# Optimization experiments

Measured on AMD Instinct MI355X. Metric: run time of the kernel, lower is better.

Reference implementation:

```python
import jax, jax.numpy as jnp
import numpy as np

B, T, D_IN, H, D_OUT = 64, 512, 512, 1024, 512

def setup_inputs() -> dict:
    key = jax.random.key(0)
    ks = jax.random.split(key, 8)
    s = 0.02  # weight init scale to keep gates in a sane range
    return {
        "x": jax.random.normal(ks[0], (B, T, D_IN), jnp.float32),
        "hx": jax.random.normal(ks[1], (B, H), jnp.float32) * 0.1,
        "cx": jax.random.normal(ks[2], (B, H), jnp.float32) * 0.1,
        "yx": jax.nn.softmax(jax.random.normal(ks[3], (B, D_OUT), jnp.float32), axis=-1),
        "Wi": jax.random.normal(ks[4], (4 * H, D_IN), jnp.float32) * s,
        "bi": jnp.zeros((4 * H,), jnp.float32),
        "Wh": jax.random.normal(ks[5], (4 * H, H), jnp.float32) * s,
        "bh": jnp.zeros((4 * H,), jnp.float32),
        "Wp": jax.random.normal(ks[6], (4 * H, D_OUT), jnp.float32) * s,
        "bp": jnp.zeros((4 * H,), jnp.float32),
        "Wo": jax.random.normal(ks[7], (D_OUT, H), jnp.float32) * s,
        "bo": jnp.zeros((D_OUT,), jnp.float32),
    }

def reference(x, hx, cx, yx, Wi, bi, Wh, bh, Wp, bp, Wo, bo):
    # Precompute input projections for all timesteps: [T, B, 4H]
    xg = jnp.einsum("btd,gd->tbg", x, Wi) + bi

    def step(carry, xg_t):
        h, c, y = carry
        gates = xg_t + h @ Wh.T + bh + y @ Wp.T + bp  # [B, 4H]
        i_g, f_g, g_g, o_g = jnp.split(gates, 4, axis=-1)
        i_g = jax.nn.sigmoid(i_g)
        f_g = jax.nn.sigmoid(f_g)
        g_g = jnp.tanh(g_g)
        o_g = jax.nn.sigmoid(o_g)
        c_new = f_g * c + i_g * g_g
        h_new = o_g * jnp.tanh(c_new)
        y_new = jax.nn.softmax(h_new @ Wo.T + bo, axis=-1)  # softmax feedback
        return (h_new, c_new, y_new), (h_new, y_new)

    (hT, cT, yT), (h_seq, y_seq) = jax.lax.scan(step, (hx, cx, yx), xg)
    output = jnp.transpose(h_seq, (1, 0, 2))       # [B, T, H]   (batch_first)
    output_peep = jnp.transpose(y_seq, (1, 0, 2))  # [B, T, D_OUT]
    return output, output_peep, hT, cT, yT
```

## Files before the change

kernel.cpp:

```cpp
#include <hip/hip_runtime.h>
#include <math.h>


typedef __bf16 bf16;
typedef bf16  bf16x8 __attribute__((ext_vector_type(8)));
typedef float f32x4  __attribute__((ext_vector_type(4)));
typedef unsigned long long u64;
typedef unsigned int u32;

#define B_    64
#define T_    512
#define DIN_  512
#define H_    1024
#define DOUT_ 512
#define NBLK  256
#define NTHR  512
#define GBLK  64
#define GROWS 16

__device__ __forceinline__ bf16x8 ld8f(const float* __restrict__ p) {
  const float4 a = *(const float4*)p;
  const float4 b = *(const float4*)(p + 4);
  bf16x8 r;
  r[0]=(bf16)a.x; r[1]=(bf16)a.y; r[2]=(bf16)a.z; r[3]=(bf16)a.w;
  r[4]=(bf16)b.x; r[5]=(bf16)b.y; r[6]=(bf16)b.z; r[7]=(bf16)b.w;
  return r;
}

__device__ __forceinline__ float sigm(float x){ return 1.f/(1.f+__expf(-x)); }

__device__ __forceinline__ void st_u64(void* p, u64 v) {
  __hip_atomic_store((u64*)p, v, __ATOMIC_RELAXED, __HIP_MEMORY_SCOPE_AGENT);
}
__device__ __forceinline__ u64 ld_u64(const void* p) {
  return __hip_atomic_load((const u64*)p, __ATOMIC_RELAXED, __HIP_MEMORY_SCOPE_AGENT);
}
__device__ __forceinline__ void st_u32(void* p, u32 v) {
  __hip_atomic_store((u32*)p, v, __ATOMIC_RELAXED, __HIP_MEMORY_SCOPE_AGENT);
}
__device__ __forceinline__ u32 ld_u32(const void* p) {
  return __hip_atomic_load((const u32*)p, __ATOMIC_RELAXED, __HIP_MEMORY_SCOPE_AGENT);
}
__device__ __forceinline__ void st_f32(float* p, float v) {
  __hip_atomic_store(p, v, __ATOMIC_RELAXED, __HIP_MEMORY_SCOPE_AGENT);
}
__device__ __forceinline__ float ld_f32(const float* p) {
  return __hip_atomic_load(p, __ATOMIC_RELAXED, __HIP_MEMORY_SCOPE_AGENT);
}
__device__ __forceinline__ bf16x8 ldh16(const bf16* p) {
  union { u64 q[2]; bf16x8 v; } u;
  u.q[0] = ld_u64(p);
  u.q[1] = ld_u64(p + 4);
  return u.v;
}

__device__ __forceinline__ void gsync(u32* fl, int myn, u32 ep) {
  asm volatile("s_waitcnt vmcnt(0)" ::: "memory");
  __syncthreads();
  const int tid = threadIdx.x;
  if (tid == 0) st_u32(fl + (size_t)myn * 32, ep);
  if (tid < GBLK) {
    const u32* f = fl + (size_t)tid * 32;
    while (ld_u32(f) < ep) __builtin_amdgcn_s_sleep(1);
  }
  __syncthreads();
}

__global__ __launch_bounds__(NTHR, 2)
void lstm_kernel(const float* __restrict__ x,  const float* __restrict__ hx,
                 const float* __restrict__ cx, const float* __restrict__ yx,
                 const float* __restrict__ Wi, const float* __restrict__ bi,
                 const float* __restrict__ Wh, const float* __restrict__ bh,
                 const float* __restrict__ Wp, const float* __restrict__ bp,
                 const float* __restrict__ Wo, const float* __restrict__ bo,
                 float* __restrict__ out, char* __restrict__ ws) {
  u32*   flags  = (u32*)ws;
  float* rowsum = (float*)(ws + 33024);
  bf16*  hbuf   = (bf16*)(ws + 36864);
  bf16*  ebuf   = (bf16*)(ws + 36864 + 2*B_*H_*2);

  float* out_h  = out;
  float* out_y  = out + (size_t)B_*T_*H_;
  float* out_hT = out_y + (size_t)B_*T_*DOUT_;
  float* out_cT = out_hT + B_*H_;
  float* out_yT = out_cT + B_*H_;

  const int tid  = threadIdx.x;
  const int bid  = blockIdx.x;
  const int g    = bid & 3;
  const int n    = bid >> 2;
  const int w    = tid >> 6;
  const int lane = tid & 63;
  const int quad = lane >> 4;
  const int ln15 = lane & 15;
  const int r0   = g * GROWS;

  u32* gfl = flags + (size_t)(g * GBLK) * 32;

  __shared__ float lred[8][16][66];
  __shared__ float lds2[8][16][17];
  __shared__ bf16  hstage[16][16];
  __shared__ bf16  estage[16][16];

  bf16* h0 = hbuf;
  bf16* h1 = hbuf + (size_t)B_*H_;

  bf16x8 wfrag[8][4];
  {
    #pragma unroll
    for (int ks = 0; ks < 8; ++ks) {
      #pragma unroll
      for (int ns = 0; ns < 4; ++ns) {
        const int grow = ns*H_ + n*16 + ln15;
        const int kabs = w*256 + ks*32 + quad*8;
        const float* p;
        if      (w < 2) p = Wi + (size_t)grow * DIN_  + kabs;
        else if (w < 6) p = Wh + (size_t)grow * H_    + (kabs - 512);
        else            p = Wp + (size_t)grow * DOUT_ + (kabs - 1536);
        wfrag[ks][ns] = ld8f(p);
      }
    }
  }
  bf16x8 wofrag[4];
  if (n < 32) {
    #pragma unroll
    for (int ks = 0; ks < 4; ++ks)
      wofrag[ks] = ld8f(Wo + (size_t)(n*16 + ln15)*H_ + w*128 + ks*32 + quad*8);
  }

  const int crow = (tid >> 4) & 15;
  const int chl  = tid & 15;
  const int cb   = r0 + crow;
  const int ccol = n*16 + chl;
  float c = 0.f;
  float bias4[4];
  if (tid < 256) {
    c = cx[(size_t)cb * H_ + ccol];
    #pragma unroll
    for (int gg = 0; gg < 4; ++gg) {
      const int grow = gg*H_ + ccol;
      bias4[gg] = bi[grow] + bh[grow] + bp[grow];
    }
  }

  {
    const int idx = n * NTHR + tid;
    if (idx < GROWS*H_/2) {
      const int row = idx >> 9, c2 = (idx & 511) * 2;
      const float* hp = hx + (size_t)(r0 + row)*H_ + c2;
      union { u32 q; bf16 h[2]; } u;
      u.h[0] = (bf16)hp[0]; u.h[1] = (bf16)hp[1];
      st_u32(h0 + (size_t)(r0 + row)*H_ + c2, u.q);
    } else if (idx < GROWS*H_/2 + GROWS*DOUT_/2) {
      const int j = idx - GROWS*H_/2;
      const int row = j >> 8, c2 = (j & 255) * 2;
      const float* yp = yx + (size_t)(r0 + row)*DOUT_ + c2;
      union { u32 q; bf16 h[2]; } u;
      u.h[0] = (bf16)yp[0]; u.h[1] = (bf16)yp[1];
      st_u32(ebuf + (size_t)B_*DOUT_ + (size_t)(r0 + row)*DOUT_ + c2, u.q);
    }
    if (n == 0 && tid < GROWS) {
      st_f32(rowsum + 64 + r0 + tid, 1.0f);
      st_f32(rowsum + r0 + tid, 0.0f);
    }
  }

  u32 ep = 0;
  gsync(gfl, n, ++ep);

  for (int t = 0; t < T_; ++t) {
    bf16*       hbR = (t & 1) ? h1 : h0;
    bf16*       hbW = (t & 1) ? h0 : h1;
    const bf16* EbR = ebuf + (size_t)(((t + 1) & 1)) * B_ * DOUT_;
    bf16*       EbW = ebuf + (size_t)((t & 1)) * B_ * DOUT_;
    const float* rsPrev = rowsum + ((t & 1) ^ 1) * 64;
    float*       rsCur  = rowsum + (t & 1) * 64;

    if (n == 0 && tid < GROWS) st_f32(rsCur + r0 + tid, 0.f);

    f32x4 acc[4];
    #pragma unroll
    for (int j = 0; j < 4; ++j) acc[j] = f32x4{0.f, 0.f, 0.f, 0.f};

    if (w < 2) {
      const float* base = x + ((size_t)(r0 + ln15)*T_ + t)*DIN_ + w*256 + quad*8;
      #pragma unroll
      for (int ks = 0; ks < 8; ++ks) {
        const bf16x8 a = ld8f(base + ks*32);
        #pragma unroll
        for (int ns = 0; ns < 4; ++ns)
          acc[ns] = __builtin_amdgcn_mfma_f32_16x16x32_bf16(a, wfrag[ks][ns], acc[ns], 0,0,0);
      }
    } else if (w < 6) {
      const bf16* base = hbR + (size_t)(r0 + ln15)*H_ + (w-2)*256 + quad*8;
      #pragma unroll
      for (int ks = 0; ks < 8; ++ks) {
        const bf16x8 a = ldh16(base + ks*32);
        #pragma unroll
        for (int ns = 0; ns < 4; ++ns)
          acc[ns] = __builtin_amdgcn_mfma_f32_16x16x32_bf16(a, wfrag[ks][ns], acc[ns], 0,0,0);
      }
    } else {
      const bf16* base = EbR + (size_t)(r0 + ln15)*DOUT_ + (w-6)*256 + quad*8;
      float rinv4[4];
      #pragma unroll
      for (int r = 0; r < 4; ++r)
        rinv4[r] = 1.f / ld_f32(rsPrev + r0 + quad*4 + r);
      #pragma unroll
      for (int ks = 0; ks < 8; ++ks) {
        const bf16x8 a = ldh16(base + ks*32);
        #pragma unroll
        for (int ns = 0; ns < 4; ++ns)
          acc[ns] = __builtin_amdgcn_mfma_f32_16x16x32_bf16(a, wfrag[ks][ns], acc[ns], 0,0,0);
      }
      #pragma unroll
      for (int ns = 0; ns < 4; ++ns)
        #pragma unroll
        for (int r = 0; r < 4; ++r)
          acc[ns][r] *= rinv4[r];
    }

    #pragma unroll
    for (int ns = 0; ns < 4; ++ns)
      #pragma unroll
      for (int r = 0; r < 4; ++r)
        lred[w][quad*4 + r][ns*16 + ln15] = acc[ns][r];
    __syncthreads();

    if (tid < 256) {
      float v[4];
      #pragma unroll
      for (int gg = 0; gg < 4; ++gg) {
        float s = bias4[gg];
        #pragma unroll
        for (int ww = 0; ww < 8; ++ww) s += lred[ww][crow][gg*16 + chl];
        v[gg] = s;
      }
      const float ig = sigm(v[0]);
      const float fg = sigm(v[1]);
      const float gv = tanhf(v[2]);
      const float og = sigm(v[3]);
      c = fg * c + ig * gv;
      const float hn = og * tanhf(c);
      out_h[((size_t)cb * T_ + t) * H_ + ccol] = hn;
      hstage[crow][chl] = (bf16)hn;
      if (t == T_ - 1) {
        out_hT[(size_t)cb * H_ + ccol] = hn;
        out_cT[(size_t)cb * H_ + ccol] = c;
      }
    }
    __syncthreads();
    if (tid < 64) {
      const int row = tid >> 2, c4 = (tid & 3) * 4;
      union { u64 q; bf16 h[4]; } u;
      #pragma unroll
      for (int j = 0; j < 4; ++j) u.h[j] = hstage[row][c4 + j];
      st_u64(hbW + (size_t)(r0 + row)*H_ + n*16 + c4, u.q);
    }

    gsync(gfl, n, ++ep);

    if (n < 32) {
      f32x4 a2 = f32x4{0.f, 0.f, 0.f, 0.f};
      const bf16* base = hbW + (size_t)(r0 + ln15)*H_ + w*128 + quad*8;
      #pragma unroll
      for (int ks = 0; ks < 4; ++ks) {
        const bf16x8 af = ldh16(base + ks*32);
        a2 = __builtin_amdgcn_mfma_f32_16x16x32_bf16(af, wofrag[ks], a2, 0,0,0);
      }
      #pragma unroll
      for (int r = 0; r < 4; ++r)
        lds2[w][quad*4 + r][ln15] = a2[r];
      __syncthreads();
      if (tid < 256) {
        const int row = tid >> 4, col = tid & 15;
        float s = bo[n*16 + col];
        #pragma unroll
        for (int ww = 0; ww < 8; ++ww) s += lds2[ww][row][col];
        const float e = __expf(s);
        estage[row][col] = (bf16)e;
        lds2[0][row][col] = e;
      }
      __syncthreads();
      if (tid < 64) {
        const int row = tid >> 2, c4 = (tid & 3) * 4;
        union { u64 q; bf16 h[4]; } u;
        #pragma unroll
        for (int j = 0; j < 4; ++j) u.h[j] = estage[row][c4 + j];
        st_u64(EbW + (size_t)(r0 + row)*DOUT_ + n*16 + c4, u.q);
      }
      if (tid < 16) {
        float s = 0.f;
        #pragma unroll
        for (int j = 0; j < 16; ++j) s += lds2[0][tid][j];
        __hip_atomic_fetch_add(rsCur + r0 + tid, s,
                               __ATOMIC_RELAXED, __HIP_MEMORY_SCOPE_AGENT);
      }
    } else if (n < 48 && t > 0) {
      if (tid < 256) {
        const int b_ = r0 + (n - 32);
        const float rinv = 1.f / ld_f32(rsPrev + b_);
        union { u32 q; bf16 h[2]; } u;
        u.q = ld_u32(EbR + (size_t)b_*DOUT_ + tid*2);
        float2 o;
        o.x = (float)u.h[0] * rinv;
        o.y = (float)u.h[1] * rinv;
        *(float2*)(out_y + ((size_t)b_*T_ + (t - 1))*DOUT_ + tid*2) = o;
      }
    }

    gsync(gfl, n, ++ep);
  }

  if (n >= 32 && n < 48 && tid < 256) {
    const int b_ = r0 + (n - 32);
    const float* rsLast = rowsum + ((T_ - 1) & 1) * 64;
    const float rinv = 1.f / ld_f32(rsLast + b_);
    const bf16* ebL = ebuf + (size_t)((T_ - 1) & 1) * B_ * DOUT_;
    union { u32 q; bf16 h[2]; } u;
    u.q = ld_u32(ebL + (size_t)b_*DOUT_ + tid*2);
    float2 o;
    o.x = (float)u.h[0] * rinv;
    o.y = (float)u.h[1] * rinv;
    *(float2*)(out_y + ((size_t)b_*T_ + (T_ - 1))*DOUT_ + tid*2) = o;
    *(float2*)(out_yT + (size_t)b_*DOUT_ + tid*2) = o;
  }
}

extern "C" void kernel_launch(void* const* d_in, const int* in_sizes, int n_in,
                              void* d_out, int out_size, void* d_ws, size_t ws_size,
                              hipStream_t stream) {
  hipMemsetAsync(d_ws, 0, 36864, stream);
  hipLaunchKernelGGL(lstm_kernel, dim3(NBLK), dim3(NTHR), 0, stream,
                     (const float*)d_in[0],  (const float*)d_in[1],
                     (const float*)d_in[2],  (const float*)d_in[3],
                     (const float*)d_in[4],  (const float*)d_in[5],
                     (const float*)d_in[6],  (const float*)d_in[7],
                     (const float*)d_in[8],  (const float*)d_in[9],
                     (const float*)d_in[10], (const float*)d_in[11],
                     (float*)d_out, (char*)d_ws);
}
```

Before: 6.017 ms.

## Fuse output projection into gate step via atomic logit accumulation, one barrier per step

Each block now multiplies its own 16 new hidden columns by the matching slice of Wo and atomically adds partial logits into a triple-buffered fp32 logits array, which is pre-seeded with the bias. This removes the second grid-wide barrier in every timestep. The exponential and the row sum of the softmax move into the consumer warps of the next step, with normalisation applied after the matmul. The cost is many fp32 atomics to global memory per step and redundant exp work across blocks, and the atomic accumulation order is non-deterministic.

Result: slower. 7.253 ms (+20.5%).

```diff
diff --git a/kernel.cpp b/kernel.cpp
--- a/kernel.cpp
+++ b/kernel.cpp
@@ -44,26 +44,14 @@
 __device__ __forceinline__ void st_f32(float* p, float v) {
   __hip_atomic_store(p, v, __ATOMIC_RELAXED, __HIP_MEMORY_SCOPE_AGENT);
 }
-__device__ __forceinline__ float ld_f32(const float* p) {
-  return __hip_atomic_load(p, __ATOMIC_RELAXED, __HIP_MEMORY_SCOPE_AGENT);
+__device__ __forceinline__ void at_addf(float* p, float v) {
+  __hip_atomic_fetch_add(p, v, __ATOMIC_RELAXED, __HIP_MEMORY_SCOPE_AGENT);
 }
 __device__ __forceinline__ bf16x8 ldh16(const bf16* p) {
   union { u64 q[2]; bf16x8 v; } u;
   u.q[0] = ld_u64(p);
   u.q[1] = ld_u64(p + 4);
   return u.v;
-}
-
-__device__ __forceinline__ void gsync(u32* fl, int myn, u32 ep) {
-  asm volatile("s_waitcnt vmcnt(0)" ::: "memory");
-  __syncthreads();
-  const int tid = threadIdx.x;
-  if (tid == 0) st_u32(fl + (size_t)myn * 32, ep);
-  if (tid < GBLK) {
-    const u32* f = fl + (size_t)tid * 32;
-    while (ld_u32(f) < ep) __builtin_amdgcn_s_sleep(1);
-  }
-  __syncthreads();
 }
 
 __global__ __launch_bounds__(NTHR, 2)
@@ -75,9 +63,8 @@
                  const float* __restrict__ Wo, const float* __restrict__ bo,
                  float* __restrict__ out, char* __restrict__ ws) {
   u32*   flags  = (u32*)ws;
-  float* rowsum = (float*)(ws + 33024);
-  bf16*  hbuf   = (bf16*)(ws + 36864);
-  bf16*  ebuf   = (bf16*)(ws + 36864 + 2*B_*H_*2);
+  float* logits = (float*)(ws + 32768);
+  bf16*  hbuf   = (bf16*)(ws + 32768 + 4*3*GROWS*DOUT_*4);
 
   float* out_h  = out;
   float* out_y  = out + (size_t)B_*T_*H_;
@@ -95,12 +82,12 @@
   const int ln15 = lane & 15;
   const int r0   = g * GROWS;
 
-  u32* gfl = flags + (size_t)(g * GBLK) * 32;
+  u32*   gfl = flags + (size_t)(g * GBLK) * 32;
+  float* lgt = logits + (size_t)g * 3 * GROWS * DOUT_;
 
   __shared__ float lred[8][16][66];
-  __shared__ float lds2[8][16][17];
   __shared__ bf16  hstage[16][16];
-  __shared__ bf16  estage[16][16];
+  __shared__ float lds_rs[2][16];
 
   bf16* h0 = hbuf;
   bf16* h1 = hbuf + (size_t)B_*H_;
@@ -121,11 +108,19 @@
       }
     }
   }
-  bf16x8 wofrag[4];
-  if (n < 32) {
-    #pragma unroll
-    for (int ks = 0; ks < 4; ++ks)
-      wofrag[ks] = ld8f(Wo + (size_t)(n*16 + ln15)*H_ + w*128 + ks*32 + quad*8);
+
+  bf16x8 wofrag2[4];
+  {
+    bf16x8 z;
+    #pragma unroll
+    for (int j = 0; j < 8; ++j) z[j] = (bf16)0.f;
+    #pragma unroll
+    for (int m = 0; m < 4; ++m) {
+      if (quad < 2)
+        wofrag2[m] = ld8f(Wo + (size_t)(w*64 + m*16 + ln15)*H_ + n*16 + quad*8);
+      else
+        wofrag2[m] = z;
+    }
   }
 
   const int crow = (tid >> 4) & 15;
@@ -143,6 +138,9 @@
     }
   }
 
+  float bo_mine = 0.f;
+  if (tid < 128) bo_mine = bo[(n*128 + tid) & (DOUT_ - 1)];
+
   {
     const int idx = n * NTHR + tid;
     if (idx < GROWS*H_/2) {
@@ -151,32 +149,28 @@
       union { u32 q; bf16 h[2]; } u;
       u.h[0] = (bf16)hp[0]; u.h[1] = (bf16)hp[1];
       st_u32(h0 + (size_t)(r0 + row)*H_ + c2, u.q);
-    } else if (idx < GROWS*H_/2 + GROWS*DOUT_/2) {
-      const int j = idx - GROWS*H_/2;
-      const int row = j >> 8, c2 = (j & 255) * 2;
-      const float* yp = yx + (size_t)(r0 + row)*DOUT_ + c2;
-      union { u32 q; bf16 h[2]; } u;
-      u.h[0] = (bf16)yp[0]; u.h[1] = (bf16)yp[1];
-      st_u32(ebuf + (size_t)B_*DOUT_ + (size_t)(r0 + row)*DOUT_ + c2, u.q);
-    }
-    if (n == 0 && tid < GROWS) {
-      st_f32(rowsum + 64 + r0 + tid, 1.0f);
-      st_f32(rowsum + r0 + tid, 0.0f);
-    }
-  }
-
-  u32 ep = 0;
-  gsync(gfl, n, ++ep);
+    }
+    if (tid < 128) st_f32(lgt + n*128 + tid, bo_mine);
+  }
+
+  u32 ep = 1;
+  {
+    asm volatile("s_waitcnt vmcnt(0)" ::: "memory");
+    __syncthreads();
+    if (tid == 0) st_u32(gfl + (size_t)n * 32, ep);
+    if (tid < GBLK) {
+      const u32* f = gfl + (size_t)tid * 32;
+      while (ld_u32(f) < ep) __builtin_amdgcn_s_sleep(1);
+    }
+    __syncthreads();
+  }
 
   for (int t = 0; t < T_; ++t) {
     bf16*       hbR = (t & 1) ? h1 : h0;
     bf16*       hbW = (t & 1) ? h0 : h1;
-    const bf16* EbR = ebuf + (size_t)(((t + 1) & 1)) * B_ * DOUT_;
-    bf16*       EbW = ebuf + (size_t)((t & 1)) * B_ * DOUT_;
-    const float* rsPrev = rowsum + ((t & 1) ^ 1) * 64;
-    float*       rsCur  = rowsum + (t & 1) * 64;
-
-    if (n == 0 && tid < GROWS) st_f32(rsCur + r0 + tid, 0.f);
+    const float* lgtPrev = lgt + (size_t)((t + 2) % 3) * GROWS * DOUT_;
+    float*       lgtCur  = lgt + (size_t)(t % 3)       * GROWS * DOUT_;
+    float*       lgtNext = lgt + (size_t)((t + 1) % 3) * GROWS * DOUT_;
 
     f32x4 acc[4];
     #pragma unroll
@@ -201,23 +195,36 @@
           acc[ns] = __builtin_amdgcn_mfma_f32_16x16x32_bf16(a, wfrag[ks][ns], acc[ns], 0,0,0);
       }
     } else {
-      const bf16* base = EbR + (size_t)(r0 + ln15)*DOUT_ + (w-6)*256 + quad*8;
-      float rinv4[4];
-      #pragma unroll
-      for (int r = 0; r < 4; ++r)
-        rinv4[r] = 1.f / ld_f32(rsPrev + r0 + quad*4 + r);
+      float rs = 0.f;
       #pragma unroll
       for (int ks = 0; ks < 8; ++ks) {
-        const bf16x8 a = ldh16(base + ks*32);
+        const int col = (w-6)*256 + ks*32 + quad*8;
+        float pv[8];
+        if (t == 0) {
+          const float* yp = yx + (size_t)(r0 + ln15)*DOUT_ + col;
+          const float4 a4 = *(const float4*)yp;
+          const float4 b4 = *(const float4*)(yp + 4);
+          pv[0]=a4.x; pv[1]=a4.y; pv[2]=a4.z; pv[3]=a4.w;
+          pv[4]=b4.x; pv[5]=b4.y; pv[6]=b4.z; pv[7]=b4.w;
+        } else {
+          const float* pp = lgtPrev + ln15*DOUT_ + col;
+          #pragma unroll
+          for (int u2 = 0; u2 < 4; ++u2) {
+            union { u64 q; float f[2]; } ua; ua.q = ld_u64(pp + u2*2);
+            pv[u2*2]   = __expf(ua.f[0]);
+            pv[u2*2+1] = __expf(ua.f[1]);
+          }
+        }
+        bf16x8 a;
+        #pragma unroll
+        for (int j = 0; j < 8; ++j) { rs += pv[j]; a[j] = (bf16)pv[j]; }
         #pragma unroll
         for (int ns = 0; ns < 4; ++ns)
           acc[ns] = __builtin_amdgcn_mfma_f32_16x16x32_bf16(a, wfrag[ks][ns], acc[ns], 0,0,0);
       }
-      #pragma unroll
-      for (int ns = 0; ns < 4; ++ns)
-        #pragma unroll
-        for (int r = 0; r < 4; ++r)
-          acc[ns][r] *= rinv4[r];
+      rs += __shfl_xor(rs, 16);
+      rs += __shfl_xor(rs, 32);
+      if (quad == 0) lds_rs[w-6][ln15] = rs;
     }
 
     #pragma unroll
@@ -227,110 +234,129 @@
         lred[w][quad*4 + r][ns*16 + ln15] = acc[ns][r];
     __syncthreads();
 
+    float rinv_y = 1.f;
+    if (w >= 6 && t > 0)
+      rinv_y = 1.f / (lds_rs[0][ln15] + lds_rs[1][ln15]);
+
+    float hn = 0.f;
     if (tid < 256) {
+      const float rsum = lds_rs[0][crow] + lds_rs[1][crow];
+      const float rinv = (t == 0) ? 1.f : 1.f / rsum;
       float v[4];
       #pragma unroll
       for (int gg = 0; gg < 4; ++gg) {
-        float s = bias4[gg];
-        #pragma unroll
-        for (int ww = 0; ww < 8; ++ww) s += lred[ww][crow][gg*16 + chl];
-        v[gg] = s;
+        const int cl = gg*16 + chl;
+        const float s05 = lred[0][crow][cl] + lred[1][crow][cl] + lred[2][crow][cl]
+                        + lred[3][crow][cl] + lred[4][crow][cl] + lred[5][crow][cl];
+        const float se  = lred[6][crow][cl] + lred[7][crow][cl];
+        v[gg] = s05 + se * rinv + bias4[gg];
       }
       const float ig = sigm(v[0]);
       const float fg = sigm(v[1]);
       const float gv = tanhf(v[2]);
       const float og = sigm(v[3]);
       c = fg * c + ig * gv;
-      const float hn = og * tanhf(c);
+      hn = og * tanhf(c);
+      hstage[crow][chl] = (bf16)hn;
+    }
+    __syncthreads();
+
+    {
+      bf16x8 a2;
+      #pragma unroll
+      for (int j = 0; j < 8; ++j) a2[j] = (bf16)0.f;
+      if (quad < 2) a2 = *(const bf16x8*)&hstage[ln15][quad*8];
+      #pragma unroll
+      for (int m = 0; m < 4; ++m) {
+        f32x4 d = f32x4{0.f, 0.f, 0.f, 0.f};
+        d = __builtin_amdgcn_mfma_f32_16x16x32_bf16(a2, wofrag2[m], d, 0,0,0);
+        #pragma unroll
+        for (int r = 0; r < 4; ++r)
+          at_addf(lgtCur + (quad*4 + r)*DOUT_ + w*64 + m*16 + ln15, d[r]);
+      }
+    }
+
+    if (tid < 64) {
+      const int row = tid >> 2, c4 = (tid & 3) * 4;
+      union { u64 q; bf16 h[4]; } u;
+      #pragma unroll
+      for (int j = 0; j < 4; ++j) u.h[j] = hstage[row][c4 + j];
+      st_u64(hbW + (size_t)(r0 + row)*H_ + n*16 + c4, u.q);
+    }
+    if (tid < 128) st_f32(lgtNext + n*128 + tid, bo_mine);
+
+    asm volatile("s_waitcnt vmcnt(0)" ::: "memory");
+    __syncthreads();
+    ++ep;
+    if (tid == 0) st_u32(gfl + (size_t)n * 32, ep);
+
+    if (tid < 256) {
       out_h[((size_t)cb * T_ + t) * H_ + ccol] = hn;
-      hstage[crow][chl] = (bf16)hn;
       if (t == T_ - 1) {
         out_hT[(size_t)cb * H_ + ccol] = hn;
         out_cT[(size_t)cb * H_ + ccol] = c;
       }
     }
-    __syncthreads();
-    if (tid < 64) {
-      const int row = tid >> 2, c4 = (tid & 3) * 4;
-      union { u64 q; bf16 h[4]; } u;
-      #pragma unroll
-      for (int j = 0; j < 4; ++j) u.h[j] = hstage[row][c4 + j];
-      st_u64(hbW + (size_t)(r0 + row)*H_ + n*16 + c4, u.q);
-    }
-
-    gsync(gfl, n, ++ep);
-
-    if (n < 32) {
-      f32x4 a2 = f32x4{0.f, 0.f, 0.f, 0.f};
-      const bf16* base = hbW + (size_t)(r0 + ln15)*H_ + w*128 + quad*8;
-      #pragma unroll
-      for (int ks = 0; ks < 4; ++ks) {
-        const bf16x8 af = ldh16(base + ks*32);
-        a2 = __builtin_amdgcn_mfma_f32_16x16x32_bf16(af, wofrag[ks], a2, 0,0,0);
-      }
-      #pragma unroll
-      for (int r = 0; r < 4; ++r)
-        lds2[w][quad*4 + r][ln15] = a2[r];
-      __syncthreads();
-      if (tid < 256) {
-        const int row = tid >> 4, col = tid & 15;
-        float s = bo[n*16 + col];
-        #pragma unroll
-        for (int ww = 0; ww < 8; ++ww) s += lds2[ww][row][col];
-        const float e = __expf(s);
-        estage[row][col] = (bf16)e;
-        lds2[0][row][col] = e;
-      }
-      __syncthreads();
-      if (tid < 64) {
-        const int row = tid >> 2, c4 = (tid & 3) * 4;
-        union { u64 q; bf16 h[4]; } u;
-        #pragma unroll
-        for (int j = 0; j < 4; ++j) u.h[j] = estage[row][c4 + j];
-        st_u64(EbW + (size_t)(r0 + row)*DOUT_ + n*16 + c4, u.q);
-      }
-      if (tid < 16) {
-        float s = 0.f;
-        #pragma unroll
-        for (int j = 0; j < 16; ++j) s += lds2[0][tid][j];
-        __hip_atomic_fetch_add(rsCur + r0 + tid, s,
-                               __ATOMIC_RELAXED, __HIP_MEMORY_SCOPE_AGENT);
-      }
-    } else if (n < 48 && t > 0) {
-      if (tid < 256) {
-        const int b_ = r0 + (n - 32);
-        const float rinv = 1.f / ld_f32(rsPrev + b_);
-        union { u32 q; bf16 h[2]; } u;
-        u.q = ld_u32(EbR + (size_t)b_*DOUT_ + tid*2);
-        float2 o;
-        o.x = (float)u.h[0] * rinv;
-        o.y = (float)u.h[1] * rinv;
-        *(float2*)(out_y + ((size_t)b_*T_ + (t - 1))*DOUT_ + tid*2) = o;
-      }
-    }
-
-    gsync(gfl, n, ++ep);
-  }
-
-  if (n >= 32 && n < 48 && tid < 256) {
-    const int b_ = r0 + (n - 32);
-    const float* rsLast = rowsum + ((T_ - 1) & 1) * 64;
-    const float rinv = 1.f / ld_f32(rsLast + b_);
-    const bf16* ebL = ebuf + (size_t)((T_ - 1) & 1) * B_ * DOUT_;
-    union { u32 q; bf16 h[2]; } u;
-    u.q = ld_u32(ebL + (size_t)b_*DOUT_ + tid*2);
-    float2 o;
-    o.x = (float)u.h[0] * rinv;
-    o.y = (float)u.h[1] * rinv;
-    *(float2*)(out_y + ((size_t)b_*T_ + (T_ - 1))*DOUT_ + tid*2) = o;
-    *(float2*)(out_yT + (size_t)b_*DOUT_ + tid*2) = o;
+    if (w >= 6 && n < 8 && t > 0) {
+      const int col = (w-6)*256 + n*32 + quad*8;
+      const float* pp = lgtPrev + ln15*DOUT_ + col;
+      float* oy = out_y + ((size_t)(r0 + ln15)*T_ + (t - 1))*DOUT_ + col;
+      #pragma unroll
+      for (int u2 = 0; u2 < 4; ++u2) {
+        union { u64 q; float f[2]; } ua; ua.q = ld_u64(pp + u2*2);
+        oy[u2*2]   = __expf(ua.f[0]) * rinv_y;
+        oy[u2*2+1] = __expf(ua.f[1]) * rinv_y;
+      }
+    }
+
+    if (tid < GBLK) {
+      const u32* f = gfl + (size_t)tid * 32;
+      while (ld_u32(f) < ep) __builtin_amdgcn_s_sleep(1);
+    }
+    __syncthreads();
+  }
+
+  if (n < 8) {
+    const float* lp = lgt + (size_t)((T_ + 2) % 3) * GROWS * DOUT_;
+    if (w >= 6) {
+      float rs = 0.f;
+      #pragma unroll
+      for (int ks = 0; ks < 8; ++ks) {
+        const int col = (w-6)*256 + ks*32 + quad*8;
+        const float* pp = lp + ln15*DOUT_ + col;
+        #pragma unroll
+        for (int u2 = 0; u2 < 4; ++u2) {
+          union { u64 q; float f[2]; } ua; ua.q = ld_u64(pp + u2*2);
+          rs += __expf(ua.f[0]) + __expf(ua.f[1]);
+        }
+      }
+      rs += __shfl_xor(rs, 16);
+      rs += __shfl_xor(rs, 32);
+      if (quad == 0) lds_rs[w-6][ln15] = rs;
+    }
+    __syncthreads();
+    if (w >= 6) {
+      const float rinv = 1.f / (lds_rs[0][ln15] + lds_rs[1][ln15]);
+      const int col = (w-6)*256 + n*32 + quad*8;
+      const float* pp = lp + ln15*DOUT_ + col;
+      float* oy  = out_y  + ((size_t)(r0 + ln15)*T_ + (T_ - 1))*DOUT_ + col;
+      float* oyT = out_yT + (size_t)(r0 + ln15)*DOUT_ + col;
+      #pragma unroll
+      for (int u2 = 0; u2 < 4; ++u2) {
+        union { u64 q; float f[2]; } ua; ua.q = ld_u64(pp + u2*2);
+        const float y0 = __expf(ua.f[0]) * rinv;
+        const float y1 = __expf(ua.f[1]) * rinv;
+        oy[u2*2] = y0;  oy[u2*2+1] = y1;
+        oyT[u2*2] = y0; oyT[u2*2+1] = y1;
+      }
+    }
   }
 }
 
 extern "C" void kernel_launch(void* const* d_in, const int* in_sizes, int n_in,
                               void* d_out, int out_size, void* d_ws, size_t ws_size,
                               hipStream_t stream) {
-  hipMemsetAsync(d_ws, 0, 36864, stream);
+  (void)hipMemsetAsync(d_ws, 0, 32768, stream);
   hipLaunchKernelGGL(lstm_kernel, dim3(NBLK), dim3(NTHR), 0, stream,
                      (const float*)d_in[0],  (const float*)d_in[1],
                      (const float*)d_in[2],  (const float*)d_in[3],
```
